# Performance work log

Measured on AMD Instinct MI355X. Metric: run time of the kernel, lower is better.

The kernel has to match this reference:

```python
import jax, jax.numpy as jnp
import numpy as np

B, S, HID = 2, 2048, 2048
NH, NKV, HD = 32, 8, 64
EPS = 1e-6
SCALE = HD ** -0.5


def rms_norm(x, w, eps=EPS):
    xf = x.astype(jnp.float32)
    var = jnp.mean(xf * xf, axis=-1, keepdims=True)
    return (w * (xf * jax.lax.rsqrt(var + eps))).astype(x.dtype)


def rotate_half(x):
    x1, x2 = jnp.split(x, 2, axis=-1)
    return jnp.concatenate((-x2, x1), axis=-1)


def setup_inputs() -> dict:
    key = jax.random.key(0)
    ks = jax.random.split(key, 8)
    hidden_states = jax.random.normal(ks[0], (B, S, HID), jnp.float32)
    # realistic RoPE tables
    inv_freq = 1.0 / (500000.0 ** (np.arange(0, HD, 2, dtype=np.float32) / HD))
    pos = np.arange(S, dtype=np.float32)
    freqs = np.outer(pos, inv_freq)                      # [S, HD/2]
    emb = np.concatenate([freqs, freqs], axis=-1)        # [S, HD]
    cos = jnp.broadcast_to(jnp.asarray(np.cos(emb)), (B, S, HD))
    sin = jnp.broadcast_to(jnp.asarray(np.sin(emb)), (B, S, HD))
    std = HID ** -0.5
    Wq = jax.random.normal(ks[1], (NH * HD, HID), jnp.float32) * std
    Wk = jax.random.normal(ks[2], (NKV * HD, HID), jnp.float32) * std
    Wv = jax.random.normal(ks[3], (NKV * HD, HID), jnp.float32) * std
    Wo = jax.random.normal(ks[4], (HID, NH * HD), jnp.float32) * std
    q_norm_w = jnp.ones((HD,), jnp.float32)
    k_norm_w = jnp.ones((HD,), jnp.float32)
    return {"hidden_states": hidden_states, "cos": cos, "sin": sin,
            "Wq": Wq, "Wk": Wk, "Wv": Wv, "Wo": Wo,
            "q_norm_w": q_norm_w, "k_norm_w": k_norm_w}


def reference(hidden_states, cos, sin, Wq, Wk, Wv, Wo, q_norm_w, k_norm_w):
    b, s, _ = hidden_states.shape
    # QKV projections (nn.Linear: x @ W.T)
    q = (hidden_states @ Wq.T).reshape(b, s, NH, HD).transpose(0, 2, 1, 3)   # [B,NH,S,D]
    k = (hidden_states @ Wk.T).reshape(b, s, NKV, HD).transpose(0, 2, 1, 3)  # [B,NKV,S,D]
    v = (hidden_states @ Wv.T).reshape(b, s, NKV, HD).transpose(0, 2, 1, 3)
    # per-head QK RMSNorm (use_head_qk_norm=True)
    q = rms_norm(q, q_norm_w)
    k = rms_norm(k, k_norm_w)
    # RoPE, cos/sin broadcast over heads (unsqueeze dim 1)
    c = cos[:, None, :, :]
    sn = sin[:, None, :, :]
    q = q * c + rotate_half(q) * sn
    k = k * c + rotate_half(k) * sn
    # GQA: expand kv heads to query heads
    groups = NH // NKV
    k = jnp.repeat(k, groups, axis=1)
    v = jnp.repeat(v, groups, axis=1)
    # eager SDPA, causal, softmax in fp32
    scores = jnp.einsum('bhqd,bhkd->bhqk', q, k) * SCALE
    causal = jnp.tril(jnp.ones((s, s), bool))
    scores = jnp.where(causal, scores, jnp.finfo(jnp.float32).min)
    probs = jax.nn.softmax(scores.astype(jnp.float32), axis=-1).astype(q.dtype)
    attn = jnp.einsum('bhqk,bhkd->bhqd', probs, v)       # [B,NH,S,D]
    attn = attn.transpose(0, 2, 1, 3).reshape(b, s, NH * HD)
    return attn @ Wo.T
```

## Files before the change

### kernel.cpp

```cpp
#include <hip/hip_runtime.h>
#include <hip/hip_bf16.h>
#include <stdint.h>

typedef __bf16 bf16;
typedef __bf16 bf16x8 __attribute__((ext_vector_type(8)));
typedef float floatx4 __attribute__((ext_vector_type(4)));
typedef float floatx8 __attribute__((ext_vector_type(8)));

#define MFMA16(A, B, C) __builtin_amdgcn_mfma_f32_16x16x32_bf16(A, B, C, 0, 0, 0)

constexpr int Sc = 2048, HIDc = 2048, NHc = 32, NKVc = 8, HDc = 64;
constexpr float kScale = 0.125f;
constexpr float kMax = 9.0f;

__device__ __forceinline__ void async16(const bf16* g, bf16* l) {
  __builtin_amdgcn_global_load_lds(
      (const __attribute__((address_space(1))) void*)g,
      (__attribute__((address_space(3))) void*)l, 16, 0, 0);
}

__global__ __launch_bounds__(256)
void cvt5(const float* __restrict__ s0, bf16* __restrict__ d0, int n0,
          const float* __restrict__ s1, bf16* __restrict__ d1, int n1,
          const float* __restrict__ s2, bf16* __restrict__ d2, int n2,
          const float* __restrict__ s3, bf16* __restrict__ d3, int n3,
          const float* __restrict__ s4, bf16* __restrict__ d4, int n4)
{
  const float* s; bf16* d; int n;
  switch (blockIdx.y) {
    case 0: s = s0; d = d0; n = n0; break;
    case 1: s = s1; d = d1; n = n1; break;
    case 2: s = s2; d = d2; n = n2; break;
    case 3: s = s3; d = d3; n = n3; break;
    default: s = s4; d = d4; n = n4; break;
  }
  const size_t stride = (size_t)gridDim.x * blockDim.x * 8;
  for (size_t i = ((size_t)blockIdx.x * blockDim.x + threadIdx.x) * 8;
       i < (size_t)n; i += stride) {
    floatx8 f = *(const floatx8*)(s + i);
    bf16x8 o;
#pragma unroll
    for (int j = 0; j < 8; ++j) o[j] = (bf16)f[j];
    *(bf16x8*)(d + i) = o;
  }
}

template<bool CF32>
__device__ __forceinline__
void gemm_bt_async(const bf16* __restrict__ A, const bf16* __restrict__ Bw,
                   void* __restrict__ C, int N, int K, int m0, int n0,
                   bf16* As, bf16* Bs)
{
  const int tid  = threadIdx.x;
  const int lane = tid & 63;
  const int w    = tid >> 6;
  const int wm   = (w >> 1) * 64;
  const int wn   = (w & 1) * 64;
  const int r    = lane & 15;
  const int quad = lane >> 4;

  floatx4 acc[4][4] = {};

  const int seg0 = tid, seg1 = tid + 256;
  const bf16* gA0 = A  + (size_t)(m0 + (seg0 >> 2)) * K + (seg0 & 3) * 8;
  const bf16* gA1 = A  + (size_t)(m0 + (seg1 >> 2)) * K + (seg1 & 3) * 8;
  const bf16* gB0 = Bw + (size_t)(n0 + (seg0 >> 2)) * K + (seg0 & 3) * 8;
  const bf16* gB1 = Bw + (size_t)(n0 + (seg1 >> 2)) * K + (seg1 & 3) * 8;
  bf16* lA0 = As + seg0 * 8; bf16* lA1 = As + seg1 * 8;
  bf16* lB0 = Bs + seg0 * 8; bf16* lB1 = Bs + seg1 * 8;

  for (int k0 = 0; k0 < K; k0 += 32) {
    __syncthreads();
    async16(gA0 + k0, lA0);
    async16(gA1 + k0, lA1);
    async16(gB0 + k0, lB0);
    async16(gB1 + k0, lB1);
    __syncthreads();

    bf16x8 af[4], bfr[4];
#pragma unroll
    for (int mt = 0; mt < 4; ++mt)
      af[mt] = *(const bf16x8*)(As + (wm + mt * 16 + r) * 32 + quad * 8);
#pragma unroll
    for (int nt = 0; nt < 4; ++nt)
      bfr[nt] = *(const bf16x8*)(Bs + (wn + nt * 16 + r) * 32 + quad * 8);
#pragma unroll
    for (int mt = 0; mt < 4; ++mt)
#pragma unroll
      for (int nt = 0; nt < 4; ++nt)
        acc[mt][nt] = MFMA16(af[mt], bfr[nt], acc[mt][nt]);
  }

#pragma unroll
  for (int mt = 0; mt < 4; ++mt) {
#pragma unroll
    for (int nt = 0; nt < 4; ++nt) {
      const int row = m0 + wm + mt * 16 + quad * 4;
      const int col = n0 + wn + nt * 16 + r;
#pragma unroll
      for (int reg = 0; reg < 4; ++reg) {
        const size_t ci = (size_t)(row + reg) * N + col;
        const float v = acc[mt][nt][reg];
        if constexpr (CF32) ((float*)C)[ci] = v;
        else                ((bf16*)C)[ci] = (bf16)v;
      }
    }
  }
}

__global__ __launch_bounds__(256, 3)
void qkv_gemm(const bf16* __restrict__ hs,
              const bf16* __restrict__ Wq, const bf16* __restrict__ Wk,
              const bf16* __restrict__ Wv,
              bf16* __restrict__ q_ws, bf16* __restrict__ k_ws,
              bf16* __restrict__ v_ws)
{
  __shared__ bf16 As[128 * 32];
  __shared__ bf16 Bs[128 * 32];
  const int by = blockIdx.y;
  const bf16* Bw; bf16* C; int N, n0;
  if (by < 16)      { Bw = Wq; C = q_ws; N = 2048; n0 = by * 128; }
  else if (by < 20) { Bw = Wk; C = k_ws; N = 512;  n0 = (by - 16) * 128; }
  else              { Bw = Wv; C = v_ws; N = 512;  n0 = (by - 20) * 128; }
  gemm_bt_async<false>(hs, Bw, C, N, HIDc, blockIdx.x * 128, n0, As, Bs);
}

__global__ __launch_bounds__(256, 3)
void o_gemm(const bf16* __restrict__ a_ws, const bf16* __restrict__ Wo,
            float* __restrict__ out)
{
  __shared__ bf16 As[128 * 32];
  __shared__ bf16 Bs[128 * 32];
  gemm_bt_async<true>(a_ws, Wo, out, HIDc, NHc * HDc,
                      blockIdx.x * 128, blockIdx.y * 128, As, Bs);
}

__global__ __launch_bounds__(256)
void norm_rope_k(bf16* __restrict__ kk, const float* __restrict__ kw,
                 const float* __restrict__ cp, const float* __restrict__ sp)
{
  const int m = blockIdx.x;
  const int lane = threadIdx.x & 63;
  const int w = threadIdx.x >> 6;
  const float c  = cp[(size_t)m * 64 + lane];
  const float s  = sp[(size_t)m * 64 + lane];
  const float wk = kw[lane];
  for (int h = w; h < NKVc; h += 4) {
    bf16* p = kk + (size_t)m * (NKVc * HDc) + h * HDc + lane;
    float x = (float)*p;
    float ss = x * x;
#pragma unroll
    for (int off = 1; off < 64; off <<= 1) ss += __shfl_xor(ss, off);
    const float rr = rsqrtf(ss * (1.0f / 64.0f) + 1e-6f);
    const float y = wk * x * rr;
    const float partner = __shfl_xor(y, 32);
    const float rot = (lane < 32) ? -partner : partner;
    *p = (bf16)(y * c + rot * s);
  }
}

__global__ __launch_bounds__(256)
void v_transpose(const bf16* __restrict__ v, bf16* __restrict__ vt)
{
  __shared__ bf16 Ts[64 * 64];
  const int bi  = blockIdx.x;
  const int st  = bi & 31;
  const int kvh = (bi >> 5) & 7;
  const int b   = bi >> 8;
  const int tid = threadIdx.x;
  for (int seg = tid; seg < 512; seg += 256) {
    const int sr = seg >> 3, dc = (seg & 7) * 8;
    bf16x8 xv = *(const bf16x8*)(v + (size_t)(b * Sc + st * 64 + sr) * (NKVc * HDc)
                                   + kvh * HDc + dc);
#pragma unroll
    for (int i = 0; i < 8; ++i)
      Ts[(dc + i) * 64 + (sr ^ dc)] = xv[i];
  }
  __syncthreads();
  for (int seg = tid; seg < 512; seg += 256) {
    const int d = seg >> 3, sc = (seg & 7) * 8;
    bf16x8 yv = *(const bf16x8*)(&Ts[d * 64 + (sc ^ (d & 56))]);
    *(bf16x8*)(vt + ((size_t)((b * NKVc + kvh) * 64 + d)) * Sc + st * 64 + sc) = yv;
  }
}

__global__ __launch_bounds__(256, 4)
void attn_fwd(const bf16* __restrict__ q, const bf16* __restrict__ k,
              const bf16* __restrict__ vt, bf16* __restrict__ o,
              const float* __restrict__ qw, const float* __restrict__ cp,
              const float* __restrict__ sp)
{
  __shared__ bf16 Ks[64 * 64];
  __shared__ bf16 Vs[64 * 64];
  __shared__ bf16 Ps[4][16 * 72];

  const int bi  = blockIdx.x;
  const int pa  = bi & 15;
  const int h   = (bi >> 4) & 31;
  const int b   = bi >> 9;
  const int kvh = h >> 2;
  const int tid = threadIdx.x, lane = tid & 63, w = tid >> 6;
  const int r = lane & 15, quad = lane >> 4;
  const int qt0 = 31 - pa, qt1 = pa;

  const floatx8 w0 = *(const floatx8*)(qw + quad * 8);
  const floatx8 w1 = *(const floatx8*)(qw + 32 + quad * 8);
  bf16x8 qf[2][2];
#pragma unroll
  for (int t = 0; t < 2; ++t) {
    const int qt = t == 0 ? qt0 : qt1;
    const int m = b * Sc + qt * 64 + w * 16 + r;
    const bf16* qp = q + (size_t)m * (NHc * HDc) + h * HDc + quad * 8;
    bf16x8 x0 = *(const bf16x8*)qp;
    bf16x8 x1 = *(const bf16x8*)(qp + 32);
    float ss = 0.f;
#pragma unroll
    for (int i = 0; i < 8; ++i)
      ss += (float)x0[i] * (float)x0[i] + (float)x1[i] * (float)x1[i];
    ss += __shfl_xor(ss, 16);
    ss += __shfl_xor(ss, 32);
    const float rq = rsqrtf(ss * (1.0f / 64.0f) + 1e-6f) * kScale;
    const floatx8 c0 = *(const floatx8*)(cp + (size_t)m * 64 + quad * 8);
    const floatx8 c1 = *(const floatx8*)(cp + (size_t)m * 64 + 32 + quad * 8);
    const floatx8 s0 = *(const floatx8*)(sp + (size_t)m * 64 + quad * 8);
    const floatx8 s1 = *(const floatx8*)(sp + (size_t)m * 64 + 32 + quad * 8);
    bf16x8 y0v, y1v;
#pragma unroll
    for (int i = 0; i < 8; ++i) {
      const float y0 = (float)x0[i] * rq * w0[i];
      const float y1 = (float)x1[i] * rq * w1[i];
      y0v[i] = (bf16)(y0 * c0[i] - y1 * s0[i]);
      y1v[i] = (bf16)(y1 * c1[i] + y0 * s1[i]);
    }
    qf[t][0] = y0v; qf[t][1] = y1v;
  }

  floatx4 accO[2][4] = {};
  float lsum[2][4] = {};

  const int kvr = tid >> 3;
  const int cA  = (tid & 7) * 8;
  const int cx  = cA ^ (8 * (kvr & 7));
  const int xk  = 8 * (r & 15 & 7);

  const bf16* kp = k + (size_t)b * Sc * (NKVc * HDc) + kvh * HDc;
  const bf16* vp = vt + ((size_t)((b * NKVc + kvh) * 64)) * Sc;

  for (int j = 0; j <= qt0; ++j) {
    __syncthreads();
    {
      const bf16* kj = kp + (size_t)j * 64 * (NKVc * HDc);
      const bf16* vj = vp + j * 64;
      async16(kj + (size_t)kvr * (NKVc * HDc) + cx, Ks + tid * 8);
      async16(kj + (size_t)(kvr + 32) * (NKVc * HDc) + cx, Ks + (tid + 256) * 8);
      async16(vj + (size_t)kvr * Sc + cx, Vs + tid * 8);
      async16(vj + (size_t)(kvr + 32) * Sc + cx, Vs + (tid + 256) * 8);
    }
    __syncthreads();

#pragma unroll
    for (int t = 0; t < 2; ++t) {
      if (t == 1 && j > qt1) continue;
      const int qt = t == 0 ? qt0 : qt1;

      floatx4 sa[4];
#pragma unroll
      for (int nt = 0; nt < 4; ++nt) sa[nt] = floatx4{0.f, 0.f, 0.f, 0.f};
#pragma unroll
      for (int nt = 0; nt < 4; ++nt) {
        const int kv = nt * 16 + r;
        const bf16x8 kb0 = *(const bf16x8*)(&Ks[kv * 64 + ((quad * 8) ^ xk)]);
        const bf16x8 kb1 = *(const bf16x8*)(&Ks[kv * 64 + ((quad * 8 + 32) ^ xk)]);
        sa[nt] = MFMA16(qf[t][0], kb0, sa[nt]);
        sa[nt] = MFMA16(qf[t][1], kb1, sa[nt]);
      }

      const int maskbase = (j == qt) ? (w * 16 + quad * 4) : 1000;
#pragma unroll
      for (int reg = 0; reg < 4; ++reg) {
#pragma unroll
        for (int nt = 0; nt < 4; ++nt) {
          const float p = (nt * 16 + r <= maskbase + reg)
                              ? __expf(sa[nt][reg] - kMax) : 0.f;
          lsum[t][reg] += p;
          Ps[w][(quad * 4 + reg) * 72 + nt * 16 + r] = (bf16)p;
        }
      }

      const bf16x8 pa0 = *(const bf16x8*)(&Ps[w][r * 72 + quad * 8]);
      const bf16x8 pa1 = *(const bf16x8*)(&Ps[w][r * 72 + 32 + quad * 8]);
#pragma unroll
      for (int dt = 0; dt < 4; ++dt) {
        const int d = dt * 16 + r;
        const bf16x8 vb0 = *(const bf16x8*)(&Vs[d * 64 + ((quad * 8) ^ xk)]);
        const bf16x8 vb1 = *(const bf16x8*)(&Vs[d * 64 + ((quad * 8 + 32) ^ xk)]);
        accO[t][dt] = MFMA16(pa0, vb0, accO[t][dt]);
        accO[t][dt] = MFMA16(pa1, vb1, accO[t][dt]);
      }
    }
  }

#pragma unroll
  for (int t = 0; t < 2; ++t) {
    const int qt = t == 0 ? qt0 : qt1;
#pragma unroll
    for (int reg = 0; reg < 4; ++reg) {
      float l = lsum[t][reg];
#pragma unroll
      for (int off = 1; off < 16; off <<= 1) l += __shfl_xor(l, off);
      const float inv = 1.0f / l;
      const size_t row = (size_t)(b * Sc + qt * 64 + w * 16 + quad * 4 + reg);
#pragma unroll
      for (int dt = 0; dt < 4; ++dt)
        o[row * (NHc * HDc) + h * HDc + dt * 16 + r] = (bf16)(accO[t][dt][reg] * inv);
    }
  }
}

extern "C" void kernel_launch(void* const* d_in, const int* in_sizes, int n_in,
                              void* d_out, int out_size, void* d_ws, size_t ws_size,
                              hipStream_t stream)
{
  const float* hs = (const float*)d_in[0];
  const float* cp = (const float*)d_in[1];
  const float* sp = (const float*)d_in[2];
  const float* Wq = (const float*)d_in[3];
  const float* Wk = (const float*)d_in[4];
  const float* Wv = (const float*)d_in[5];
  const float* Wo = (const float*)d_in[6];
  const float* qw = (const float*)d_in[7];
  const float* kw = (const float*)d_in[8];
  float* out = (float*)d_out;

  char* ws = (char*)d_ws;
  bf16* q_ws  = (bf16*)ws;
  bf16* k_ws  = (bf16*)(ws + (16u << 20));
  bf16* v_ws  = (bf16*)(ws + (20u << 20));
  bf16* vt_ws = (bf16*)(ws + (24u << 20));
  bf16* hs_b  = (bf16*)(ws + (28u << 20));
  bf16* Wq_b  = (bf16*)(ws + (44u << 20));
  bf16* Wk_b  = (bf16*)(ws + (52u << 20));
  bf16* Wv_b  = (bf16*)(ws + (54u << 20));
  bf16* Wo_b  = (bf16*)(ws + (56u << 20));
  bf16* a_ws  = q_ws;

  dim3 blk(256);
  cvt5<<<dim3(256, 5), blk, 0, stream>>>(
      hs, hs_b, 4096 * 2048, Wq, Wq_b, 2048 * 2048, Wk, Wk_b, 512 * 2048,
      Wv, Wv_b, 512 * 2048, Wo, Wo_b, 2048 * 2048);
  qkv_gemm<<<dim3(32, 24), blk, 0, stream>>>(hs_b, Wq_b, Wk_b, Wv_b,
                                             q_ws, k_ws, v_ws);
  norm_rope_k<<<dim3(4096), blk, 0, stream>>>(k_ws, kw, cp, sp);
  v_transpose<<<dim3(512), blk, 0, stream>>>(v_ws, vt_ws);
  attn_fwd<<<dim3(1024), blk, 0, stream>>>(q_ws, k_ws, vt_ws, a_ws, qw, cp, sp);
  o_gemm<<<dim3(32, 16), blk, 0, stream>>>(a_ws, Wo_b, out);
}
```

Before: 304.7 us.

## Rewrite projection GEMMs with 8-wave larger tiles and double-buffered async LDS pipeline

```diff
diff --git a/kernel.cpp b/kernel.cpp
--- a/kernel.cpp
+++ b/kernel.cpp
@@ -45,94 +45,143 @@
   }
 }
 
-template<bool CF32>
+template<int BM, int BN, bool CF32>
 __device__ __forceinline__
-void gemm_bt_async(const bf16* __restrict__ A, const bf16* __restrict__ Bw,
-                   void* __restrict__ C, int N, int K, int m0, int n0,
-                   bf16* As, bf16* Bs)
-{
+void gemm8p(const bf16* __restrict__ A, const bf16* __restrict__ Bw,
+            void* __restrict__ C, int N, int K, int m0, int n0,
+            bf16* __restrict__ lds)
+{
+  constexpr int MR2  = BM / 64;
+  constexpr int ALD  = BM / 128;
+  constexpr int BLD  = BN / 128;
+  constexpr int AH   = BM * 32;
+  constexpr int BH   = BN * 32;
+  constexpr int GATE = ALD + BLD;
+
   const int tid  = threadIdx.x;
   const int lane = tid & 63;
   const int w    = tid >> 6;
-  const int wm   = (w >> 1) * 64;
-  const int wn   = (w & 1) * 64;
   const int r    = lane & 15;
   const int quad = lane >> 4;
-
-  floatx4 acc[4][4] = {};
-
-  const int seg0 = tid, seg1 = tid + 256;
-  const bf16* gA0 = A  + (size_t)(m0 + (seg0 >> 2)) * K + (seg0 & 3) * 8;
-  const bf16* gA1 = A  + (size_t)(m0 + (seg1 >> 2)) * K + (seg1 & 3) * 8;
-  const bf16* gB0 = Bw + (size_t)(n0 + (seg0 >> 2)) * K + (seg0 & 3) * 8;
-  const bf16* gB1 = Bw + (size_t)(n0 + (seg1 >> 2)) * K + (seg1 & 3) * 8;
-  bf16* lA0 = As + seg0 * 8; bf16* lA1 = As + seg1 * 8;
-  bf16* lB0 = Bs + seg0 * 8; bf16* lB1 = Bs + seg1 * 8;
-
-  for (int k0 = 0; k0 < K; k0 += 32) {
-    __syncthreads();
-    async16(gA0 + k0, lA0);
-    async16(gA1 + k0, lA1);
-    async16(gB0 + k0, lB0);
-    async16(gB1 + k0, lB1);
-    __syncthreads();
-
-    bf16x8 af[4], bfr[4];
-#pragma unroll
-    for (int mt = 0; mt < 4; ++mt)
-      af[mt] = *(const bf16x8*)(As + (wm + mt * 16 + r) * 32 + quad * 8);
-#pragma unroll
-    for (int nt = 0; nt < 4; ++nt)
-      bfr[nt] = *(const bf16x8*)(Bs + (wn + nt * 16 + r) * 32 + quad * 8);
-#pragma unroll
-    for (int mt = 0; mt < 4; ++mt)
-#pragma unroll
-      for (int nt = 0; nt < 4; ++nt)
-        acc[mt][nt] = MFMA16(af[mt], bfr[nt], acc[mt][nt]);
-  }
-
-#pragma unroll
-  for (int mt = 0; mt < 4; ++mt) {
+  const int wm   = w >> 2;
+  const int wn   = w & 3;
+  const int NT   = K >> 6;
+
+  const bf16* gA[ALD]; const bf16* gB[BLD];
+#pragma unroll
+  for (int i = 0; i < ALD; ++i) {
+    const int ch = i * 512 + tid;
+    gA[i] = A + (size_t)(m0 + (ch >> 2)) * K + (ch & 3) * 8;
+  }
+#pragma unroll
+  for (int i = 0; i < BLD; ++i) {
+    const int ch = i * 512 + tid;
+    gB[i] = Bw + (size_t)(n0 + (ch >> 2)) * K + (ch & 3) * 8;
+  }
+
+  auto stA = [&](int kt, int s, int kk) {
+    bf16* dst = lds + (s * 2 + kk) * AH + tid * 8;
+#pragma unroll
+    for (int i = 0; i < ALD; ++i)
+      async16(gA[i] + kt * 64 + kk * 32, dst + i * 4096);
+  };
+  auto stB = [&](int kt, int s, int kk) {
+    bf16* dst = lds + 4 * AH + (s * 2 + kk) * BH + tid * 8;
+#pragma unroll
+    for (int i = 0; i < BLD; ++i)
+      async16(gB[i] + kt * 64 + kk * 32, dst + i * 4096);
+  };
+
+  const int aoff = (wm * (BM / 2) + r) * 32 + quad * 8;
+  const int boff = (wn * 64 + r) * 32 + quad * 8;
+
+  floatx4 acc[2 * MR2][4] = {};
+  bf16x8 a[MR2], b[4];
+
+#define LDB(S, KK) do { const bf16* _p = lds + 4 * AH + ((S) * 2 + (KK)) * BH + boff; \
+  _Pragma("unroll") for (int n2 = 0; n2 < 4; ++n2) b[n2] = *(const bf16x8*)(_p + n2 * 512); } while (0)
+#define LDA(S, KK, MH) do { const bf16* _p = lds + ((S) * 2 + (KK)) * AH + aoff + (MH) * (MR2 * 512); \
+  _Pragma("unroll") for (int m2 = 0; m2 < MR2; ++m2) a[m2] = *(const bf16x8*)(_p + m2 * 512); } while (0)
+#define MM(MH) do { __builtin_amdgcn_s_setprio(1); \
+  _Pragma("unroll") for (int m2 = 0; m2 < MR2; ++m2) \
+    _Pragma("unroll") for (int n2 = 0; n2 < 4; ++n2) \
+      acc[(MH) * MR2 + m2][n2] = MFMA16(a[m2], b[n2], acc[(MH) * MR2 + m2][n2]); \
+  __builtin_amdgcn_s_setprio(0); } while (0)
+#define BAR() asm volatile("s_barrier" ::: "memory")
+#define GATEW() do { if constexpr (GATE == 4) asm volatile("s_waitcnt vmcnt(4)" ::: "memory"); \
+                     else                     asm volatile("s_waitcnt vmcnt(3)" ::: "memory"); } while (0)
+
+  stA(0, 0, 0); stB(0, 0, 0); stA(0, 0, 1); stB(0, 0, 1);
+  stA(1, 1, 0); stB(1, 1, 0);
+  GATEW(); BAR();
+
+  for (int t = 0; t < NT; ++t) {
+    const int s = t & 1;
+    LDB(s, 0); LDA(s, 0, 0);
+    if (t + 1 < NT) stA(t + 1, s ^ 1, 1);
+    BAR(); MM(0); BAR();
+    LDA(s, 0, 1);
+    if (t + 1 < NT) stB(t + 1, s ^ 1, 1);
+    BAR(); MM(1); BAR();
+    LDB(s, 1); LDA(s, 1, 0);
+    if (t + 2 < NT) stA(t + 2, s, 0);
+    BAR(); MM(0); BAR();
+    LDA(s, 1, 1);
+    if (t + 2 < NT) stB(t + 2, s, 0);
+    BAR(); MM(1);
+    GATEW(); BAR();
+  }
+
+#undef LDB
+#undef LDA
+#undef MM
+#undef BAR
+#undef GATEW
+
+#pragma unroll
+  for (int mt = 0; mt < 2 * MR2; ++mt) {
 #pragma unroll
     for (int nt = 0; nt < 4; ++nt) {
-      const int row = m0 + wm + mt * 16 + quad * 4;
-      const int col = n0 + wn + nt * 16 + r;
-#pragma unroll
-      for (int reg = 0; reg < 4; ++reg) {
-        const size_t ci = (size_t)(row + reg) * N + col;
-        const float v = acc[mt][nt][reg];
+      const int row = m0 + wm * (BM / 2) + mt * 16 + quad * 4;
+      const int col = n0 + wn * 64 + nt * 16 + r;
+#pragma unroll
+      for (int g = 0; g < 4; ++g) {
+        const size_t ci = (size_t)(row + g) * N + col;
+        const float v = acc[mt][nt][g];
         if constexpr (CF32) ((float*)C)[ci] = v;
-        else                ((bf16*)C)[ci] = (bf16)v;
+        else                ((bf16*)C)[ci]  = (bf16)v;
       }
     }
   }
 }
 
-__global__ __launch_bounds__(256, 3)
-void qkv_gemm(const bf16* __restrict__ hs,
-              const bf16* __restrict__ Wq, const bf16* __restrict__ Wk,
-              const bf16* __restrict__ Wv,
-              bf16* __restrict__ q_ws, bf16* __restrict__ k_ws,
-              bf16* __restrict__ v_ws)
-{
-  __shared__ bf16 As[128 * 32];
-  __shared__ bf16 Bs[128 * 32];
-  const int by = blockIdx.y;
+__global__ __launch_bounds__(512, 2)
+void qkv_gemm8(const bf16* __restrict__ hs,
+               const bf16* __restrict__ Wq, const bf16* __restrict__ Wk,
+               const bf16* __restrict__ Wv,
+               bf16* __restrict__ q_ws, bf16* __restrict__ k_ws,
+               bf16* __restrict__ v_ws)
+{
+  __shared__ bf16 lds[2 * 2 * (256 + 256) * 32];
+  const int wg  = blockIdx.x;
+  const int swz = (wg & 7) * 24 + (wg >> 3);
+  const int mi  = swz / 12, ni = swz % 12;
   const bf16* Bw; bf16* C; int N, n0;
-  if (by < 16)      { Bw = Wq; C = q_ws; N = 2048; n0 = by * 128; }
-  else if (by < 20) { Bw = Wk; C = k_ws; N = 512;  n0 = (by - 16) * 128; }
-  else              { Bw = Wv; C = v_ws; N = 512;  n0 = (by - 20) * 128; }
-  gemm_bt_async<false>(hs, Bw, C, N, HIDc, blockIdx.x * 128, n0, As, Bs);
-}
-
-__global__ __launch_bounds__(256, 3)
-void o_gemm(const bf16* __restrict__ a_ws, const bf16* __restrict__ Wo,
-            float* __restrict__ out)
-{
-  __shared__ bf16 As[128 * 32];
-  __shared__ bf16 Bs[128 * 32];
-  gemm_bt_async<true>(a_ws, Wo, out, HIDc, NHc * HDc,
-                      blockIdx.x * 128, blockIdx.y * 128, As, Bs);
+  if (ni < 8)       { Bw = Wq; C = q_ws; N = 2048; n0 = ni * 256; }
+  else if (ni < 10) { Bw = Wk; C = k_ws; N = 512;  n0 = (ni - 8) * 256; }
+  else              { Bw = Wv; C = v_ws; N = 512;  n0 = (ni - 10) * 256; }
+  gemm8p<256, 256, false>(hs, Bw, C, N, HIDc, mi * 256, n0, lds);
+}
+
+__global__ __launch_bounds__(512, 2)
+void o_gemm8(const bf16* __restrict__ a_ws, const bf16* __restrict__ Wo,
+             float* __restrict__ out)
+{
+  __shared__ bf16 lds[2 * 2 * (128 + 256) * 32];
+  const int wg  = blockIdx.x;
+  const int swz = (wg & 7) * 32 + (wg >> 3);
+  const int mi  = swz >> 3, ni = swz & 7;
+  gemm8p<128, 256, true>(a_ws, Wo, out, HIDc, NHc * HDc, mi * 128, ni * 256, lds);
 }
 
 __global__ __launch_bounds__(256)
@@ -348,10 +397,10 @@
   cvt5<<<dim3(256, 5), blk, 0, stream>>>(
       hs, hs_b, 4096 * 2048, Wq, Wq_b, 2048 * 2048, Wk, Wk_b, 512 * 2048,
       Wv, Wv_b, 512 * 2048, Wo, Wo_b, 2048 * 2048);
-  qkv_gemm<<<dim3(32, 24), blk, 0, stream>>>(hs_b, Wq_b, Wk_b, Wv_b,
-                                             q_ws, k_ws, v_ws);
+  qkv_gemm8<<<dim3(192), dim3(512), 0, stream>>>(hs_b, Wq_b, Wk_b, Wv_b,
+                                                 q_ws, k_ws, v_ws);
   norm_rope_k<<<dim3(4096), blk, 0, stream>>>(k_ws, kw, cp, sp);
   v_transpose<<<dim3(512), blk, 0, stream>>>(v_ws, vt_ws);
   attn_fwd<<<dim3(1024), blk, 0, stream>>>(q_ws, k_ws, vt_ws, a_ws, qw, cp, sp);
-  o_gemm<<<dim3(32, 16), blk, 0, stream>>>(a_ws, Wo_b, out);
-}
+  o_gemm8<<<dim3(256), dim3(512), 0, stream>>>(a_ws, Wo_b, out);
+}
```

After: 302.2 us. No clear change (-0.8%).
